# Optimization experiments

Measured on AMD Instinct MI355X. Metric: run time of the kernel, lower is better.

Reference implementation:

```python
import jax, jax.numpy as jnp
import numpy as np
import math

B, S, D = 2, 2048, 1024
H, KV, HD = 16, 4, 64
N_REP = H // KV
ROPE_THETA = 1.0e6


def _rope_tables(seq_len, head_dim, theta):
    inv_freq = 1.0 / (theta ** (np.arange(0, head_dim, 2, dtype=np.float32) / head_dim))
    t = np.arange(seq_len, dtype=np.float32)
    freqs = np.outer(t, inv_freq)                      # [S, HD/2]
    emb = np.concatenate([freqs, freqs], axis=-1)      # [S, HD]
    return jnp.asarray(np.cos(emb)), jnp.asarray(np.sin(emb))


def setup_inputs() -> dict:
    key = jax.random.key(0)
    ks = jax.random.split(key, 6)
    cos, sin = _rope_tables(S, HD, ROPE_THETA)
    scale = 0.02
    return {
        "x": jax.random.normal(ks[0], (B, S, D), dtype=jnp.float32),
        "cos": cos,
        "sin": sin,
        "Wq": jax.random.normal(ks[1], (D, H * HD), dtype=jnp.float32) * scale,
        "Wk": jax.random.normal(ks[2], (D, KV * HD), dtype=jnp.float32) * scale,
        "Wv": jax.random.normal(ks[3], (D, KV * HD), dtype=jnp.float32) * scale,
        "Wo": jax.random.normal(ks[4], (H * HD, D), dtype=jnp.float32) * scale,
    }


def _rotate_half(u):
    u1, u2 = u[..., : HD // 2], u[..., HD // 2 :]
    return jnp.concatenate([-u2, u1], axis=-1)


def reference(x, cos, sin, Wq, Wk, Wv, Wo):
    bsz, seq_len, _ = x.shape
    q = (x @ Wq).reshape(bsz, seq_len, H, HD)   # [B,S,H,HD]
    k = (x @ Wk).reshape(bsz, seq_len, KV, HD)  # [B,S,KV,HD]
    v = (x @ Wv).reshape(bsz, seq_len, KV, HD)

    # RoPE: cos/sin [S,HD] broadcast over batch and heads (unsqueeze_dim=1)
    c = cos[:seq_len][None, :, None, :]
    s = sin[:seq_len][None, :, None, :]
    q = q * c + _rotate_half(q) * s
    k = k * c + _rotate_half(k) * s

    # repeat_kv: expand KV heads groupwise to H heads
    k = jnp.repeat(k, N_REP, axis=2)  # [B,S,H,HD]
    v = jnp.repeat(v, N_REP, axis=2)

    q = q.transpose(0, 2, 1, 3)  # [B,H,S,HD]
    k = k.transpose(0, 2, 1, 3)
    v = v.transpose(0, 2, 1, 3)

    scores = jnp.einsum("bhqd,bhkd->bhqk", q, k) / math.sqrt(HD)
    causal = jnp.tril(jnp.ones((seq_len, seq_len), dtype=bool))
    scores = jnp.where(causal[None, None], scores, jnp.finfo(jnp.float32).min)
    probs = jax.nn.softmax(scores.astype(jnp.float32), axis=-1).astype(x.dtype)

    out = jnp.einsum("bhqk,bhkd->bhqd", probs, v)        # [B,H,S,HD]
    out = out.transpose(0, 2, 1, 3).reshape(bsz, seq_len, H * HD)
    return out @ Wo
```

## Files before the change

### kernel.cpp

```cpp
#include <hip/hip_runtime.h>

#define SS 2048
#define NH 16
#define NKV 4
#define HD 64

typedef __bf16 bf16;
typedef __bf16 bf16x8 __attribute__((ext_vector_type(8)));
typedef float f32x4 __attribute__((ext_vector_type(4)));

#define SM_SCALE 0.18033688011f

__device__ __forceinline__ void gl_lds16(const bf16* g, bf16* l) {
    __builtin_amdgcn_global_load_lds((const __attribute__((address_space(1))) void*)g,
                                     (__attribute__((address_space(3))) void*)l, 16, 0, 0);
}

__global__ __launch_bounds__(256) void prep_kernel(
    const float* __restrict__ x, const float* __restrict__ Wq, const float* __restrict__ Wk,
    const float* __restrict__ Wv, const float* __restrict__ Wo,
    bf16* __restrict__ xb, bf16* __restrict__ wqkv_t, bf16* __restrict__ wo_t)
{
    const int blk = blockIdx.x;
    const int tid = threadIdx.x;
    if (blk >= 640) {
        const float4* xv = (const float4*)x;
        const size_t base = (size_t)(blk - 640) * 2048 + tid;
        #pragma unroll
        for (int j = 0; j < 8; ++j) {
            const float4 v = xv[base + j * 256];
            bf16* o = xb + (base + j * 256) * 4;
            o[0] = (bf16)v.x; o[1] = (bf16)v.y; o[2] = (bf16)v.z; o[3] = (bf16)v.w;
        }
        return;
    }
    const float* W; bf16* Wt; int N, n0, k0;
    if (blk < 256)      { W = Wq; Wt = wqkv_t;                       N = 1024; n0 = (blk & 15) * 64;         k0 = (blk >> 4) * 64; }
    else if (blk < 320) { W = Wk; Wt = wqkv_t + (size_t)1024 * 1024; N = 256;  n0 = ((blk - 256) & 3) * 64;  k0 = ((blk - 256) >> 2) * 64; }
    else if (blk < 384) { W = Wv; Wt = wqkv_t + (size_t)1280 * 1024; N = 256;  n0 = ((blk - 320) & 3) * 64;  k0 = ((blk - 320) >> 2) * 64; }
    else                { W = Wo; Wt = wo_t;                         N = 1024; n0 = ((blk - 384) & 15) * 64; k0 = ((blk - 384) >> 4) * 64; }

    __shared__ float Ts[64][65];
    const int c = tid & 63, rr = tid >> 6;
    #pragma unroll
    for (int i = 0; i < 16; ++i) {
        const int kk = i * 4 + rr;
        Ts[kk][c] = W[(size_t)(k0 + kk) * N + n0 + c];
    }
    __syncthreads();
    #pragma unroll
    for (int i = 0; i < 16; ++i) {
        const int nn = i * 4 + rr;
        Wt[(size_t)(n0 + nn) * 1024 + k0 + c] = (bf16)Ts[c][nn];
    }
}

template<int EPI>
__global__ __launch_bounds__(512) void gemm_bt_kernel(
    const bf16* __restrict__ A, const bf16* __restrict__ Bt, float* __restrict__ C,
    const float* __restrict__ cosp, const float* __restrict__ sinp,
    bf16* __restrict__ qo, bf16* __restrict__ ko, bf16* __restrict__ vto,
    int M, int N, int K)
{
    __shared__ bf16 As[128 * 32];
    __shared__ bf16 Bs[128 * 32];
    const int m0 = blockIdx.x * 128, n0 = blockIdx.y * 128;
    const int tid = threadIdx.x;
    const int w = tid >> 6, lane = tid & 63, g = lane >> 4, li = lane & 15;
    const int wm = w >> 1, wn = w & 1;

    f32x4 acc[2][4];
    const f32x4 z = {0.f, 0.f, 0.f, 0.f};
    #pragma unroll
    for (int i = 0; i < 2; ++i)
        #pragma unroll
        for (int j = 0; j < 4; ++j) acc[i][j] = z;

    const int srow = tid >> 2, schunk = (tid & 3) * 8;
    const bf16* pA = A + (size_t)(m0 + srow) * K + schunk;
    const bf16* pB = Bt + (size_t)(n0 + srow) * K + schunk;
    bf16* lA = As + (size_t)w * 512;
    bf16* lB = Bs + (size_t)w * 512;

    for (int kk = 0; kk < K; kk += 32) {
        __syncthreads();
        gl_lds16(pA + kk, lA);
        gl_lds16(pB + kk, lB);
        __syncthreads();
        bf16x8 af[2], bfr[4];
        #pragma unroll
        for (int mi = 0; mi < 2; ++mi) af[mi] = *(const bf16x8*)&As[(wm * 32 + mi * 16 + li) * 32 + g * 8];
        #pragma unroll
        for (int ni = 0; ni < 4; ++ni) bfr[ni] = *(const bf16x8*)&Bs[(wn * 64 + ni * 16 + li) * 32 + g * 8];
        #pragma unroll
        for (int mi = 0; mi < 2; ++mi)
            #pragma unroll
            for (int ni = 0; ni < 4; ++ni)
                acc[mi][ni] = __builtin_amdgcn_mfma_f32_16x16x32_bf16(af[mi], bfr[ni], acc[mi][ni], 0, 0, 0);
    }

    const int row0 = m0 + wm * 32, col0 = n0 + wn * 64;
    if (EPI == 0) {
        #pragma unroll
        for (int mi = 0; mi < 2; ++mi)
            #pragma unroll
            for (int ni = 0; ni < 4; ++ni)
                #pragma unroll
                for (int r = 0; r < 4; ++r)
                    C[(size_t)(row0 + mi * 16 + g * 4 + r) * N + col0 + ni * 16 + li] = acc[mi][ni][r];
    } else {
        #pragma unroll
        for (int ni = 0; ni < 4; ++ni) {
            const int col = col0 + ni * 16 + li;
            const int d = col & 63;
            #pragma unroll
            for (int mi = 0; mi < 2; ++mi) {
                #pragma unroll
                for (int r = 0; r < 4; ++r) {
                    const int row = row0 + mi * 16 + g * 4 + r;
                    const int bb = row >> 11, s = row & 2047;
                    float val = acc[mi][ni][r];
                    if (col < 1280) {
                        const float pairv = acc[mi][ni ^ 2][r];
                        const float rot = (d < 32) ? -pairv : pairv;
                        val = val * cosp[s * 64 + d] + rot * sinp[s * 64 + d];
                    }
                    if (col < 1024) {
                        const int hh = col >> 6;
                        qo[(((size_t)bb * NH + hh) * SS + s) * HD + d] = (bf16)val;
                    } else if (col < 1280) {
                        const int kh = (col - 1024) >> 6;
                        ko[(((size_t)bb * NKV + kh) * SS + s) * HD + d] = (bf16)val;
                    } else {
                        const int kh = (col - 1280) >> 6;
                        vto[(((size_t)bb * NKV + kh) * HD + d) * SS + s] = (bf16)val;
                    }
                }
            }
        }
    }
}

#define FP 72
#define FPV 136
__global__ __launch_bounds__(256) void flash_kernel(const bf16* __restrict__ q, const bf16* __restrict__ k,
                                                    const bf16* __restrict__ vt, bf16* __restrict__ o)
{
    __shared__ bf16 Ks[128][FP];
    __shared__ bf16 Vt[64][FPV];
    __shared__ bf16 Ps[4][16][FP];

    const int blk = blockIdx.x;
    const int p = blk & 15;
    const int h = (blk >> 4) & 15;
    const int b = blk >> 8;
    const int kvh = h >> 2;
    const int tid = threadIdx.x;
    const int w = tid >> 6, lane = tid & 63, g = lane >> 4, li = lane & 15;

    const bf16* qh = q + ((size_t)b * NH + h) * SS * HD;
    const bf16* kh = k + ((size_t)b * NKV + kvh) * SS * HD;
    const bf16* vh = vt + ((size_t)b * NKV + kvh) * (size_t)HD * SS;

    bf16x8 ones;
    #pragma unroll
    for (int j = 0; j < 8; ++j) ones[j] = (bf16)1.0f;
    const f32x4 z = {0.f, 0.f, 0.f, 0.f};

    #pragma unroll
    for (int phase = 0; phase < 2; ++phase) {
        const int qt = phase ? p : (31 - p);

        const bf16* qrow = qh + (size_t)(qt * 64 + w * 16 + li) * HD;
        bf16x8 qf[2];
        qf[0] = *(const bf16x8*)(qrow + g * 8);
        qf[1] = *(const bf16x8*)(qrow + 32 + g * 8);

        f32x4 o_acc[4], l_acc;
        #pragma unroll
        for (int nt = 0; nt < 4; ++nt) o_acc[nt] = z;
        l_acc = z;

        for (int kt0 = 0; kt0 <= qt; kt0 += 2) {
            __syncthreads();
            {
                const int krow = tid >> 1, kcol = (tid & 1) * 32;
                const uint4* ks = (const uint4*)(kh + (size_t)(kt0 * 64 + krow) * HD + kcol);
                const uint4 a0 = ks[0], a1 = ks[1], a2 = ks[2], a3 = ks[3];
                *(uint4*)&Ks[krow][kcol]      = a0;
                *(uint4*)&Ks[krow][kcol + 8]  = a1;
                *(uint4*)&Ks[krow][kcol + 16] = a2;
                *(uint4*)&Ks[krow][kcol + 24] = a3;
                const int vrow = tid >> 2, vcol = (tid & 3) * 32;
                const uint4* vs = (const uint4*)(vh + (size_t)vrow * SS + kt0 * 64 + vcol);
                const uint4 c0 = vs[0], c1 = vs[1], c2 = vs[2], c3 = vs[3];
                *(uint4*)&Vt[vrow][vcol]      = c0;
                *(uint4*)&Vt[vrow][vcol + 8]  = c1;
                *(uint4*)&Vt[vrow][vcol + 16] = c2;
                *(uint4*)&Vt[vrow][vcol + 24] = c3;
            }
            __syncthreads();

            #pragma unroll
            for (int sub = 0; sub < 2; ++sub) {
                const int kt = kt0 + sub;
                if (kt > qt) break;

                f32x4 s_acc[4];
                #pragma unroll
                for (int nt = 0; nt < 4; ++nt) s_acc[nt] = z;
                #pragma unroll
                for (int t = 0; t < 2; ++t)
                    #pragma unroll
                    for (int nt = 0; nt < 4; ++nt) {
                        const bf16x8 kf = *(const bf16x8*)&Ks[sub * 64 + nt * 16 + li][t * 32 + g * 8];
                        s_acc[nt] = __builtin_amdgcn_mfma_f32_16x16x32_bf16(qf[t], kf, s_acc[nt], 0, 0, 0);
                    }

                const bool diag = (kt == qt);
                const int qr0 = qt * 64 + w * 16 + g * 4;
                #pragma unroll
                for (int nt = 0; nt < 4; ++nt) {
                    const int key = kt * 64 + nt * 16 + li;
                    #pragma unroll
                    for (int r = 0; r < 4; ++r) {
                        float sv = s_acc[nt][r] * SM_SCALE;
                        if (diag && key > qr0 + r) sv = -1e30f;
                        Ps[w][g * 4 + r][nt * 16 + li] = (bf16)exp2f(sv);
                    }
                }

                #pragma unroll
                for (int t = 0; t < 2; ++t) {
                    const bf16x8 pf = *(const bf16x8*)&Ps[w][li][t * 32 + g * 8];
                    l_acc = __builtin_amdgcn_mfma_f32_16x16x32_bf16(pf, ones, l_acc, 0, 0, 0);
                    #pragma unroll
                    for (int nt = 0; nt < 4; ++nt) {
                        const bf16x8 vf = *(const bf16x8*)&Vt[nt * 16 + li][sub * 64 + t * 32 + g * 8];
                        o_acc[nt] = __builtin_amdgcn_mfma_f32_16x16x32_bf16(pf, vf, o_acc[nt], 0, 0, 0);
                    }
                }
            }
        }

        #pragma unroll
        for (int r = 0; r < 4; ++r) {
            const float inv = 1.f / l_acc[r];
            const int s = qt * 64 + w * 16 + g * 4 + r;
            bf16* orow = o + (((size_t)b * SS + s) * NH + h) * HD;
            #pragma unroll
            for (int nt = 0; nt < 4; ++nt) orow[nt * 16 + li] = (bf16)(o_acc[nt][r] * inv);
        }
    }
}

extern "C" void kernel_launch(void* const* d_in, const int* in_sizes, int n_in,
                              void* d_out, int out_size, void* d_ws, size_t ws_size,
                              hipStream_t stream) {
    const float* x     = (const float*)d_in[0];
    const float* cos_t = (const float*)d_in[1];
    const float* sin_t = (const float*)d_in[2];
    const float* Wq    = (const float*)d_in[3];
    const float* Wk    = (const float*)d_in[4];
    const float* Wv    = (const float*)d_in[5];
    const float* Wo    = (const float*)d_in[6];
    float* out = (float*)d_out;

    char* wsb = (char*)d_ws;
    bf16* x_b    = (bf16*)(wsb);
    bf16* wqkv_t = (bf16*)(wsb + 8388608);
    bf16* wo_t   = (bf16*)(wsb + 11534336);
    bf16* q_b    = (bf16*)(wsb + 13631488);
    bf16* k_b    = (bf16*)(wsb + 22020096);
    bf16* vt_b   = (bf16*)(wsb + 24117248);
    bf16* o_b    = x_b;

    prep_kernel<<<1152, 256, 0, stream>>>(x, Wq, Wk, Wv, Wo, x_b, wqkv_t, wo_t);

    gemm_bt_kernel<2><<<dim3(32, 12), 512, 0, stream>>>(x_b, wqkv_t, nullptr, cos_t, sin_t,
                                                        q_b, k_b, vt_b, 4096, 1536, 1024);
    flash_kernel<<<512, 256, 0, stream>>>(q_b, k_b, vt_b, o_b);
    gemm_bt_kernel<0><<<dim3(32, 8), 512, 0, stream>>>(o_b, wo_t, out, nullptr, nullptr,
                                                       nullptr, nullptr, nullptr, 4096, 1024, 1024);
}
```

Measured before the change: 192.7 us.

## Retile GEMMs to 64x128 blocks, split flash work per q-tile, swizzle P LDS

The GEMM kernels now use 256-thread blocks with 64-row M tiles, which doubles the grid to fill more CUs. The flash kernel drops the paired heavy/light q-tile scheme and launches one block per q-tile, heaviest first. The softmax scale is folded into Q in the projection epilogue, so the per-score multiply is gone, and the mask check only runs on the diagonal tile. The P tile in LDS gets an XOR swizzle to cut bank conflicts. The extra launched blocks carry some per-block overhead, and the Q values rounded to bf16 after scaling differ slightly from before.

```diff
diff --git a/kernel.cpp b/kernel.cpp
--- a/kernel.cpp
+++ b/kernel.cpp
@@ -56,15 +56,15 @@
 }
 
 template<int EPI>
-__global__ __launch_bounds__(512) void gemm_bt_kernel(
+__global__ __launch_bounds__(256) void gemm_bt_kernel(
     const bf16* __restrict__ A, const bf16* __restrict__ Bt, float* __restrict__ C,
     const float* __restrict__ cosp, const float* __restrict__ sinp,
     bf16* __restrict__ qo, bf16* __restrict__ ko, bf16* __restrict__ vto,
     int M, int N, int K)
 {
-    __shared__ bf16 As[128 * 32];
+    __shared__ bf16 As[64 * 32];
     __shared__ bf16 Bs[128 * 32];
-    const int m0 = blockIdx.x * 128, n0 = blockIdx.y * 128;
+    const int m0 = blockIdx.x * 64, n0 = blockIdx.y * 128;
     const int tid = threadIdx.x;
     const int w = tid >> 6, lane = tid & 63, g = lane >> 4, li = lane & 15;
     const int wm = w >> 1, wn = w & 1;
@@ -77,15 +77,18 @@
         for (int j = 0; j < 4; ++j) acc[i][j] = z;
 
     const int srow = tid >> 2, schunk = (tid & 3) * 8;
-    const bf16* pA = A + (size_t)(m0 + srow) * K + schunk;
-    const bf16* pB = Bt + (size_t)(n0 + srow) * K + schunk;
-    bf16* lA = As + (size_t)w * 512;
-    bf16* lB = Bs + (size_t)w * 512;
+    const bf16* pA  = A  + (size_t)(m0 + srow) * K + schunk;
+    const bf16* pB0 = Bt + (size_t)(n0 + srow) * K + schunk;
+    const bf16* pB1 = Bt + (size_t)(n0 + 64 + srow) * K + schunk;
+    bf16* lA  = As + (size_t)w * 512;
+    bf16* lB0 = Bs + (size_t)w * 512;
+    bf16* lB1 = Bs + 2048 + (size_t)w * 512;
 
     for (int kk = 0; kk < K; kk += 32) {
         __syncthreads();
         gl_lds16(pA + kk, lA);
-        gl_lds16(pB + kk, lB);
+        gl_lds16(pB0 + kk, lB0);
+        gl_lds16(pB1 + kk, lB1);
         __syncthreads();
         bf16x8 af[2], bfr[4];
         #pragma unroll
@@ -127,7 +130,7 @@
                     }
                     if (col < 1024) {
                         const int hh = col >> 6;
-                        qo[(((size_t)bb * NH + hh) * SS + s) * HD + d] = (bf16)val;
+                        qo[(((size_t)bb * NH + hh) * SS + s) * HD + d] = (bf16)(val * SM_SCALE);
                     } else if (col < 1280) {
                         const int kh = (col - 1024) >> 6;
                         ko[(((size_t)bb * NKV + kh) * SS + s) * HD + d] = (bf16)val;
@@ -151,9 +154,9 @@
     __shared__ bf16 Ps[4][16][FP];
 
     const int blk = blockIdx.x;
-    const int p = blk & 15;
-    const int h = (blk >> 4) & 15;
-    const int b = blk >> 8;
+    const int qt = 31 - (blk >> 5);
+    const int h = blk & 15;
+    const int b = (blk >> 4) & 1;
     const int kvh = h >> 2;
     const int tid = threadIdx.x;
     const int w = tid >> 6, lane = tid & 63, g = lane >> 4, li = lane & 15;
@@ -167,90 +170,92 @@
     for (int j = 0; j < 8; ++j) ones[j] = (bf16)1.0f;
     const f32x4 z = {0.f, 0.f, 0.f, 0.f};
 
-    #pragma unroll
-    for (int phase = 0; phase < 2; ++phase) {
-        const int qt = phase ? p : (31 - p);
-
-        const bf16* qrow = qh + (size_t)(qt * 64 + w * 16 + li) * HD;
-        bf16x8 qf[2];
-        qf[0] = *(const bf16x8*)(qrow + g * 8);
-        qf[1] = *(const bf16x8*)(qrow + 32 + g * 8);
-
-        f32x4 o_acc[4], l_acc;
-        #pragma unroll
-        for (int nt = 0; nt < 4; ++nt) o_acc[nt] = z;
-        l_acc = z;
-
-        for (int kt0 = 0; kt0 <= qt; kt0 += 2) {
-            __syncthreads();
-            {
-                const int krow = tid >> 1, kcol = (tid & 1) * 32;
-                const uint4* ks = (const uint4*)(kh + (size_t)(kt0 * 64 + krow) * HD + kcol);
-                const uint4 a0 = ks[0], a1 = ks[1], a2 = ks[2], a3 = ks[3];
-                *(uint4*)&Ks[krow][kcol]      = a0;
-                *(uint4*)&Ks[krow][kcol + 8]  = a1;
-                *(uint4*)&Ks[krow][kcol + 16] = a2;
-                *(uint4*)&Ks[krow][kcol + 24] = a3;
-                const int vrow = tid >> 2, vcol = (tid & 3) * 32;
-                const uint4* vs = (const uint4*)(vh + (size_t)vrow * SS + kt0 * 64 + vcol);
-                const uint4 c0 = vs[0], c1 = vs[1], c2 = vs[2], c3 = vs[3];
-                *(uint4*)&Vt[vrow][vcol]      = c0;
-                *(uint4*)&Vt[vrow][vcol + 8]  = c1;
-                *(uint4*)&Vt[vrow][vcol + 16] = c2;
-                *(uint4*)&Vt[vrow][vcol + 24] = c3;
-            }
-            __syncthreads();
-
-            #pragma unroll
-            for (int sub = 0; sub < 2; ++sub) {
-                const int kt = kt0 + sub;
-                if (kt > qt) break;
-
-                f32x4 s_acc[4];
-                #pragma unroll
-                for (int nt = 0; nt < 4; ++nt) s_acc[nt] = z;
-                #pragma unroll
-                for (int t = 0; t < 2; ++t)
-                    #pragma unroll
-                    for (int nt = 0; nt < 4; ++nt) {
-                        const bf16x8 kf = *(const bf16x8*)&Ks[sub * 64 + nt * 16 + li][t * 32 + g * 8];
-                        s_acc[nt] = __builtin_amdgcn_mfma_f32_16x16x32_bf16(qf[t], kf, s_acc[nt], 0, 0, 0);
-                    }
-
-                const bool diag = (kt == qt);
+    const bf16* qrow = qh + (size_t)(qt * 64 + w * 16 + li) * HD;
+    bf16x8 qf[2];
+    qf[0] = *(const bf16x8*)(qrow + g * 8);
+    qf[1] = *(const bf16x8*)(qrow + 32 + g * 8);
+
+    f32x4 o_acc[4], l_acc;
+    #pragma unroll
+    for (int nt = 0; nt < 4; ++nt) o_acc[nt] = z;
+    l_acc = z;
+
+    for (int kt0 = 0; kt0 <= qt; kt0 += 2) {
+        __syncthreads();
+        {
+            const int krow = tid >> 1, kcol = (tid & 1) * 32;
+            const uint4* ks = (const uint4*)(kh + (size_t)(kt0 * 64 + krow) * HD + kcol);
+            const uint4 a0 = ks[0], a1 = ks[1], a2 = ks[2], a3 = ks[3];
+            *(uint4*)&Ks[krow][kcol]      = a0;
+            *(uint4*)&Ks[krow][kcol + 8]  = a1;
+            *(uint4*)&Ks[krow][kcol + 16] = a2;
+            *(uint4*)&Ks[krow][kcol + 24] = a3;
+            const int vrow = tid >> 2, vcol = (tid & 3) * 32;
+            const uint4* vs = (const uint4*)(vh + (size_t)vrow * SS + kt0 * 64 + vcol);
+            const uint4 c0 = vs[0], c1 = vs[1], c2 = vs[2], c3 = vs[3];
+            *(uint4*)&Vt[vrow][vcol]      = c0;
+            *(uint4*)&Vt[vrow][vcol + 8]  = c1;
+            *(uint4*)&Vt[vrow][vcol + 16] = c2;
+            *(uint4*)&Vt[vrow][vcol + 24] = c3;
+        }
+        __syncthreads();
+
+        #pragma unroll
+        for (int sub = 0; sub < 2; ++sub) {
+            const int kt = kt0 + sub;
+            if (kt > qt) break;
+
+            f32x4 s_acc[4];
+            #pragma unroll
+            for (int nt = 0; nt < 4; ++nt) s_acc[nt] = z;
+            #pragma unroll
+            for (int t = 0; t < 2; ++t)
+                #pragma unroll
+                for (int nt = 0; nt < 4; ++nt) {
+                    const bf16x8 kf = *(const bf16x8*)&Ks[sub * 64 + nt * 16 + li][t * 32 + g * 8];
+                    s_acc[nt] = __builtin_amdgcn_mfma_f32_16x16x32_bf16(qf[t], kf, s_acc[nt], 0, 0, 0);
+                }
+
+            if (kt == qt) {
                 const int qr0 = qt * 64 + w * 16 + g * 4;
                 #pragma unroll
                 for (int nt = 0; nt < 4; ++nt) {
                     const int key = kt * 64 + nt * 16 + li;
                     #pragma unroll
                     for (int r = 0; r < 4; ++r) {
-                        float sv = s_acc[nt][r] * SM_SCALE;
-                        if (diag && key > qr0 + r) sv = -1e30f;
-                        Ps[w][g * 4 + r][nt * 16 + li] = (bf16)exp2f(sv);
+                        float sv = s_acc[nt][r];
+                        if (key > qr0 + r) sv = -1e30f;
+                        Ps[w][g * 4 + r][(nt * 16 + li) ^ (g * 16)] = (bf16)exp2f(sv);
                     }
                 }
-
-                #pragma unroll
-                for (int t = 0; t < 2; ++t) {
-                    const bf16x8 pf = *(const bf16x8*)&Ps[w][li][t * 32 + g * 8];
-                    l_acc = __builtin_amdgcn_mfma_f32_16x16x32_bf16(pf, ones, l_acc, 0, 0, 0);
+            } else {
+                #pragma unroll
+                for (int nt = 0; nt < 4; ++nt)
                     #pragma unroll
-                    for (int nt = 0; nt < 4; ++nt) {
-                        const bf16x8 vf = *(const bf16x8*)&Vt[nt * 16 + li][sub * 64 + t * 32 + g * 8];
-                        o_acc[nt] = __builtin_amdgcn_mfma_f32_16x16x32_bf16(pf, vf, o_acc[nt], 0, 0, 0);
-                    }
-                }
+                    for (int r = 0; r < 4; ++r)
+                        Ps[w][g * 4 + r][(nt * 16 + li) ^ (g * 16)] = (bf16)exp2f(s_acc[nt][r]);
             }
-        }
-
-        #pragma unroll
-        for (int r = 0; r < 4; ++r) {
-            const float inv = 1.f / l_acc[r];
-            const int s = qt * 64 + w * 16 + g * 4 + r;
-            bf16* orow = o + (((size_t)b * SS + s) * NH + h) * HD;
-            #pragma unroll
-            for (int nt = 0; nt < 4; ++nt) orow[nt * 16 + li] = (bf16)(o_acc[nt][r] * inv);
-        }
+
+            #pragma unroll
+            for (int t = 0; t < 2; ++t) {
+                const bf16x8 pf = *(const bf16x8*)&Ps[w][li][(t * 32 + g * 8) ^ ((li >> 2) * 16)];
+                l_acc = __builtin_amdgcn_mfma_f32_16x16x32_bf16(pf, ones, l_acc, 0, 0, 0);
+                #pragma unroll
+                for (int nt = 0; nt < 4; ++nt) {
+                    const bf16x8 vf = *(const bf16x8*)&Vt[nt * 16 + li][sub * 64 + t * 32 + g * 8];
+                    o_acc[nt] = __builtin_amdgcn_mfma_f32_16x16x32_bf16(pf, vf, o_acc[nt], 0, 0, 0);
+                }
+            }
+        }
+    }
+
+    #pragma unroll
+    for (int r = 0; r < 4; ++r) {
+        const float inv = 1.f / l_acc[r];
+        const int s = qt * 64 + w * 16 + g * 4 + r;
+        bf16* orow = o + (((size_t)b * SS + s) * NH + h) * HD;
+        #pragma unroll
+        for (int nt = 0; nt < 4; ++nt) orow[nt * 16 + li] = (bf16)(o_acc[nt][r] * inv);
     }
 }
 
@@ -277,9 +282,9 @@
 
     prep_kernel<<<1152, 256, 0, stream>>>(x, Wq, Wk, Wv, Wo, x_b, wqkv_t, wo_t);
 
-    gemm_bt_kernel<2><<<dim3(32, 12), 512, 0, stream>>>(x_b, wqkv_t, nullptr, cos_t, sin_t,
+    gemm_bt_kernel<2><<<dim3(64, 12), 256, 0, stream>>>(x_b, wqkv_t, nullptr, cos_t, sin_t,
                                                         q_b, k_b, vt_b, 4096, 1536, 1024);
-    flash_kernel<<<512, 256, 0, stream>>>(q_b, k_b, vt_b, o_b);
-    gemm_bt_kernel<0><<<dim3(32, 8), 512, 0, stream>>>(o_b, wo_t, out, nullptr, nullptr,
+    flash_kernel<<<1024, 256, 0, stream>>>(q_b, k_b, vt_b, o_b);
+    gemm_bt_kernel<0><<<dim3(64, 8), 256, 0, stream>>>(o_b, wo_t, out, nullptr, nullptr,
                                                        nullptr, nullptr, nullptr, 4096, 1024, 1024);
 }
```

Measured after the change: 182.1 us. 5.5% less time.
